# Kernel optimization log

Hardware: AMD Instinct MI355X
Metric: run time of the kernel (lower is better)

Reference implementation:

```python
import jax, jax.numpy as jnp
import numpy as np

EPS = 1e-5
NEG_SLOPE = 0.1


def conv_bn_lrelu(x, w, g, b, rm, rv):
    # 1x1 conv (no bias) + BatchNorm (inference, running stats) + LeakyReLU(0.1)
    # x: [B,C,H,W], w: [O,C]
    y = jnp.einsum('bchw,oc->bohw', x, w)
    scale = g / jnp.sqrt(rv + EPS)
    y = y * scale[None, :, None, None] + (b - rm * scale)[None, :, None, None]
    return jnp.where(y >= 0, y, NEG_SLOPE * y)


def setup_inputs() -> dict:
    key = jax.random.key(0)
    ks = jax.random.split(key, 16)
    B, C, H1, W1, H2, W2 = 4, 256, 32, 32, 64, 64
    C8 = C // 8
    inp = {
        'x1': jax.random.normal(ks[0], (B, C, H1, W1), jnp.float32),
        'x2': jax.random.normal(ks[1], (B, C, H2, W2), jnp.float32),
        'wq': jax.random.normal(ks[2], (C8, C), jnp.float32) * 0.05,
        'wk': jax.random.normal(ks[3], (C8, C), jnp.float32) * 0.05,
        'wv': jax.random.normal(ks[4], (C, C), jnp.float32) * 0.05,
        'gq': jnp.ones((C8,), jnp.float32), 'bq': jnp.zeros((C8,), jnp.float32),
        'mq': jax.random.normal(ks[5], (C8,), jnp.float32) * 0.1,
        'vq': jax.random.uniform(ks[6], (C8,), jnp.float32, 0.5, 1.5),
        'gk': jnp.ones((C8,), jnp.float32), 'bk': jnp.zeros((C8,), jnp.float32),
        'mk': jax.random.normal(ks[7], (C8,), jnp.float32) * 0.1,
        'vk': jax.random.uniform(ks[8], (C8,), jnp.float32, 0.5, 1.5),
        'gv': jnp.ones((C,), jnp.float32), 'bv': jnp.zeros((C,), jnp.float32),
        'mv': jax.random.normal(ks[9], (C,), jnp.float32) * 0.1,
        'vv': jax.random.uniform(ks[10], (C,), jnp.float32, 0.5, 1.5),
        'gamma': jnp.full((1,), 0.5, jnp.float32),
    }
    return inp


def reference(x1, x2, wq, wk, wv, gq, bq, mq, vq, gk, bk, mk, vk, gv, bv, mv, vv, gamma):
    B, C, H2, W2 = x2.shape
    # bilinear upsample x1 to x2's spatial size (align_corners=False == half-pixel)
    x1u = jax.image.resize(x1, (B, C, H2, W2), method='bilinear')
    N = H2 * W2
    q = conv_bn_lrelu(x1u, wq, gq, bq, mq, vq).reshape(B, -1, N)  # [B,C8,N]
    k = conv_bn_lrelu(x2, wk, gk, bk, mk, vk).reshape(B, -1, N)   # [B,C8,N]
    v = conv_bn_lrelu(x2, wv, gv, bv, mv, vv).reshape(B, -1, N)   # [B,C,N]
    energy = jnp.einsum('bdm,bdn->bmn', q, k)                      # [B,N,N]
    attn = jax.nn.softmax(energy, axis=-1)
    out = jnp.einsum('bcn,bmn->bcm', v, attn).reshape(B, C, H2, W2)
    return gamma[0] * out + x1u
```

## Files before the change

kernel.cpp:

```cpp
#include <hip/hip_runtime.h>

#define B_ 4
#define C_ 256
#define N_ 4096
#define LOG2E 1.4426950408889634f

typedef short short8 __attribute__((ext_vector_type(8)));
typedef short short4_ __attribute__((ext_vector_type(4)));
typedef float float4v __attribute__((ext_vector_type(4)));
typedef unsigned int uint2v __attribute__((ext_vector_type(2)));
typedef unsigned int u32;

__device__ inline unsigned short f2b(float x){
  unsigned u = __builtin_bit_cast(unsigned, x);
  u = u + 0x7FFFu + ((u >> 16) & 1u);
  return (unsigned short)(u >> 16);
}

__device__ inline u32 cvtpk(float lo, float hi){
  u32 r; asm("v_cvt_pk_bf16_f32 %0, %1, %2" : "=v"(r) : "v"(lo), "v"(hi)); return r;
}

__device__ inline void gload16(const void* g, void* l){
  __builtin_amdgcn_global_load_lds((const __attribute__((address_space(1))) u32*)g,
                                   (__attribute__((address_space(3))) u32*)l, 16, 0, 0);
}

__global__ void fold_w_kernel(const float* __restrict__ wq, const float* __restrict__ wk,
    const float* __restrict__ wv,
    const float* gq, const float* bq, const float* mq, const float* vq,
    const float* gk, const float* bk, const float* mk, const float* vk,
    const float* gv, const float* bv, const float* mv, const float* vv,
    unsigned short* wqb, unsigned short* wkb, unsigned short* wvb,
    float* biasq, float* biask, float* biasv){
  int i = blockIdx.x*256 + threadIdx.x;
  int o = i >> 8;
  float sv = gv[o]*rsqrtf(vv[o]+1e-5f);
  wvb[i] = f2b(wv[i]*sv);
  if (i < 32*256){
    int oq = i >> 8;
    float sq = gq[oq]*rsqrtf(vq[oq]+1e-5f);
    wqb[i] = f2b(wq[i]*sq*LOG2E);
    float sk = gk[oq]*rsqrtf(vk[oq]+1e-5f);
    wkb[i] = f2b(wk[i]*sk);
  }
  if (i < 256) biasv[i] = bv[i] - mv[i]*(gv[i]*rsqrtf(vv[i]+1e-5f));
  if (i < 32){
    biasq[i] = (bq[i] - mq[i]*(gq[i]*rsqrtf(vq[i]+1e-5f)))*LOG2E;
    biask[i] = bk[i] - mk[i]*(gk[i]*rsqrtf(vk[i]+1e-5f));
  }
}

__global__ __launch_bounds__(256, 2)
void pre_kernel(const float* __restrict__ x1, const float* __restrict__ x2,
                const unsigned short* __restrict__ wqb,
                const unsigned short* __restrict__ wkb,
                const unsigned short* __restrict__ wvb,
                const float* __restrict__ biasq, const float* __restrict__ biask,
                const float* __restrict__ biasv,
                float* __restrict__ x1u,
                unsigned short* __restrict__ Qb, unsigned short* __restrict__ Kb,
                unsigned short* __restrict__ Vb){
  __shared__ unsigned short xt[64*260];
  int b = blockIdx.y;
  int t = threadIdx.x;
  int lane = t&63, w = t>>6, l15 = lane&15, g = lane>>4;

  if (blockIdx.z == 0){
    if (blockIdx.x >= 64) return;
    int y = blockIdx.x;
    float fy = 0.5f*y - 0.25f;
    float y0f = floorf(fy); float wy = fy - y0f;
    int y0 = max(0,min(31,(int)y0f)), y1 = max(0,min(31,(int)y0f+1));
    int x = t & 63, cg = t >> 6;
    float fx = 0.5f*x - 0.25f;
    float x0f = floorf(fx); float wx = fx - x0f;
    int x0 = max(0,min(31,(int)x0f)), x1i = max(0,min(31,(int)x0f+1));
    #pragma unroll 8
    for (int i=0;i<64;i++){
      int c = cg + i*4;
      const float* s0 = x1 + ((size_t)(b*C_ + c)*32 + y0)*32;
      const float* s1 = x1 + ((size_t)(b*C_ + c)*32 + y1)*32;
      float v00=s0[x0], v01=s0[x1i], v10=s1[x0], v11=s1[x1i];
      float v0 = v00 + wx*(v01-v00), v1 = v10 + wx*(v11-v10);
      float val = v0 + wy*(v1-v0);
      x1u[(size_t)(b*C_ + c)*N_ + y*64 + x] = val;
      xt[x*260 + c] = f2b(val);
    }
    __syncthreads();
    const unsigned short* arow = xt + (w*16+l15)*260 + g*8;
    short8 a[8];
    #pragma unroll
    for (int kk=0;kk<8;kk++){
      short4_ lo = *(const short4_*)(arow + kk*32);
      short4_ hi = *(const short4_*)(arow + kk*32 + 4);
      short8 af;
      af[0]=lo[0];af[1]=lo[1];af[2]=lo[2];af[3]=lo[3];
      af[4]=hi[0];af[5]=hi[1];af[6]=hi[2];af[7]=hi[3];
      a[kk]=af;
    }
    #pragma unroll
    for (int ot=0; ot<2; ot++){
      int o = ot*16 + l15;
      const unsigned short* wrow = wqb + o*C_ + g*8;
      float4v acc = {0.f,0.f,0.f,0.f};
      #pragma unroll
      for (int kk=0;kk<8;kk++){
        short8 bf = *(const short8*)(wrow + kk*32);
        acc = __builtin_amdgcn_mfma_f32_16x16x32_bf16(a[kk], bf, acc, 0,0,0);
      }
      float bs = biasq[o];
      #pragma unroll
      for (int r=0;r<4;r++){
        float yv = acc[r] + bs;
        yv = yv >= 0.f ? yv : 0.1f*yv;
        int m = y*64 + w*16 + g*4 + r;
        Qb[(size_t)(b*N_+m)*32 + o] = f2b(yv);
      }
    }
  } else {
    int n0 = blockIdx.x*32;
    int n = t & 31, cg = t >> 5;
    #pragma unroll 8
    for (int i=0;i<32;i++){
      int c = cg + i*8;
      float v = x2[(size_t)(b*C_ + c)*N_ + n0 + n];
      xt[n*260 + c] = f2b(v);
    }
    __syncthreads();
    int mt = w & 1;
    const unsigned short* arow = xt + (mt*16+l15)*260 + g*8;
    short8 a[8];
    #pragma unroll
    for (int kk=0;kk<8;kk++){
      short4_ lo = *(const short4_*)(arow + kk*32);
      short4_ hi = *(const short4_*)(arow + kk*32 + 4);
      short8 af;
      af[0]=lo[0];af[1]=lo[1];af[2]=lo[2];af[3]=lo[3];
      af[4]=hi[0];af[5]=hi[1];af[6]=hi[2];af[7]=hi[3];
      a[kk]=af;
    }
    if (w < 2){
      #pragma unroll
      for (int ot=0; ot<2; ot++){
        int o = ot*16 + l15;
        const unsigned short* wrow = wkb + o*C_ + g*8;
        float4v acc = {0.f,0.f,0.f,0.f};
        #pragma unroll
        for (int kk=0;kk<8;kk++){
          short8 bf = *(const short8*)(wrow + kk*32);
          acc = __builtin_amdgcn_mfma_f32_16x16x32_bf16(a[kk], bf, acc, 0,0,0);
        }
        float bs = biask[o];
        #pragma unroll
        for (int r=0;r<4;r++){
          float yv = acc[r] + bs;
          yv = yv >= 0.f ? yv : 0.1f*yv;
          int m = n0 + w*16 + g*4 + r;
          Kb[(size_t)(b*N_+m)*32 + o] = f2b(yv);
        }
      }
    }
    #pragma unroll
    for (int i=0;i<8;i++){
      int o = ((w>>1)*8 + i)*16 + l15;
      const unsigned short* wrow = wvb + (size_t)o*C_ + g*8;
      float4v acc = {0.f,0.f,0.f,0.f};
      #pragma unroll
      for (int kk=0;kk<8;kk++){
        short8 bf = *(const short8*)(wrow + kk*32);
        acc = __builtin_amdgcn_mfma_f32_16x16x32_bf16(a[kk], bf, acc, 0,0,0);
      }
      float bs = biasv[o];
      #pragma unroll
      for (int r=0;r<4;r++){
        float yv = acc[r] + bs;
        yv = yv >= 0.f ? yv : 0.1f*yv;
        int m = n0 + mt*16 + g*4 + r;
        Vb[(size_t)(b*C_ + o)*N_ + m] = f2b(yv);
      }
    }
  }
}

__global__ __launch_bounds__(512, 2)
void attn_kernel(const unsigned short* __restrict__ Qb,
                 const unsigned short* __restrict__ Kb,
                 const unsigned short* __restrict__ Vb,
                 const float* __restrict__ x1u,
                 const float* __restrict__ gamma_p,
                 float* __restrict__ out){
  __shared__ __align__(16) char smem[74528];
  int* flagsB = (int*)(smem + 73728);
  float* sclB = (float*)(smem + 73760);
  float* lst  = (float*)(smem + 74272);

  int wg = blockIdx.y*64 + blockIdx.x;
  int id = (wg & 7)*32 + (wg >> 3);
  int b = id >> 6, mblk = id & 63;
  int t = threadIdx.x, lane = t & 63, w = t >> 6;
  int l15 = lane & 15, g = lane >> 4;
  int swz = (l15 & 7) << 4;
  int cq = w & 3, ks = w >> 2;

  short8 qf{};
  if (w < 4)
    qf = *(const short8*)(Qb + (size_t)(b*N_ + mblk*64 + w*16 + l15)*32 + g*8);

  float4v acc[4][4];
  #pragma unroll
  for (int mt=0;mt<4;mt++)
    #pragma unroll
    for (int ct=0;ct<4;ct++) acc[mt][ct] = (float4v){0.f,0.f,0.f,0.f};
  float mrow = -1e30f, lrun = 0.f;
  const float4v zero4 = {0.f,0.f,0.f,0.f};

  u32 goff[4]; int loff[4];
  #pragma unroll
  for (int j=0;j<4;j++){
    int i = j*512 + t;
    int c = i >> 3, jj = i & 7;
    loff[j] = i*16;
    goff[j] = (u32)(c*(N_*2)) + (u32)((jj ^ (c & 7)) << 4);
  }
  const char* Vbyte = (const char*)Vb + (size_t)b*C_*N_*2;
  const short* kbase = (const short*)Kb + (size_t)(b*N_ + l15)*32 + g*8;

  auto stageV = [&](int tt, char* buf){
    const char* src = Vbyte + tt*128;
    #pragma unroll
    for (int j=0;j<4;j++) gload16(src + goff[j], buf + loff[j]);
  };
  auto loadK = [&](short8 (&kf)[4], int tt){
    const short* kp = kbase + (size_t)tt*64*32;
    #pragma unroll
    for (int j=0;j<4;j++) kf[j] = *(const short8*)(kp + j*512);
  };

  auto softmaxA = [&](const short8 (&kf)[4], int pdst, uint2v (&pk)[4]){
    float4v s[4];
    #pragma unroll
    for (int j=0;j<4;j++)
      s[j] = __builtin_amdgcn_mfma_f32_16x16x32_bf16(kf[j], qf, zero4, 0, 0, 0);
    float tmax = fmaxf(fmaxf(fmaxf(s[0][0],s[0][1]),fmaxf(s[0][2],s[0][3])),
               fmaxf(fmaxf(fmaxf(s[1][0],s[1][1]),fmaxf(s[1][2],s[1][3])),
               fmaxf(fmaxf(fmaxf(s[2][0],s[2][1]),fmaxf(s[2][2],s[2][3])),
                     fmaxf(fmaxf(s[3][0],s[3][1]),fmaxf(s[3][2],s[3][3])))));
    int trig = __any((tmax > mrow + 8.f) ? 1 : 0) ? 1 : 0;
    if (lane == 0) flagsB[pdst*4 + w] = trig;
    if (trig){
      float tm = fmaxf(tmax, __shfl_xor(tmax, 16));
      tm = fmaxf(tm, __shfl_xor(tm, 32));
      float mnew = fmaxf(mrow, tm);
      float sc = exp2f(mrow - mnew);
      mrow = mnew; lrun *= sc;
      if (lane < 16) sclB[pdst*64 + w*16 + l15] = sc;
    }
    #pragma unroll
    for (int j=0;j<4;j++){
      float p0 = exp2f(s[j][0]-mrow), p1 = exp2f(s[j][1]-mrow);
      float p2 = exp2f(s[j][2]-mrow), p3 = exp2f(s[j][3]-mrow);
      lrun += (p0+p1)+(p2+p3);
      pk[j] = (uint2v){cvtpk(p0, p1), cvtpk(p2, p3)};
    }
  };
  auto softmaxB = [&](uint2v (&pk)[4]){
    char* pw = smem + 65536 + w*2048 + l15*128;
    #pragma unroll
    for (int j=0;j<4;j++)
      *(uint2v*)(pw + ((j*32 + g*8) ^ swz)) = pk[j];
  };

  auto body = [&](int tt, short8 (&kC)[4], short8 (&kN)[4], uint2v (&pk)[4]){
    int pp = tt & 1;
    if (tt < 63) stageV(tt+1, smem + ((tt+1)&1)*32768);
    if (w < 4){
      loadK(kN, (tt+2) & 63);
      if (tt < 63) softmaxA(kC, (tt+1)&1, pk);
    }
    #pragma unroll
    for (int mt=0;mt<4;mt++){
      if (flagsB[pp*4 + mt]){
        float4v sv = *(float4v*)(sclB + pp*64 + mt*16 + g*4);
        #pragma unroll
        for (int ct=0;ct<4;ct++){
          acc[mt][ct][0]*=sv[0]; acc[mt][ct][1]*=sv[1];
          acc[mt][ct][2]*=sv[2]; acc[mt][ct][3]*=sv[3];
        }
      }
    }
    int ko = (ks*64 + g*16) ^ swz;
    char* vbc = smem + (tt&1)*32768;
    short8 pa[4], vf[4];
    #pragma unroll
    for (int mt=0;mt<4;mt++)
      pa[mt] = *(const short8*)(smem + 65536 + mt*2048 + l15*128 + ko);
    #pragma unroll
    for (int ct=0;ct<4;ct++)
      vf[ct] = *(const short8*)(vbc + (cq*64 + ct*16 + l15)*128 + ko);
    __builtin_amdgcn_s_setprio(1);
    #pragma unroll
    for (int mt=0;mt<4;mt++)
      #pragma unroll
      for (int ct=0;ct<4;ct++)
        acc[mt][ct] = __builtin_amdgcn_mfma_f32_16x16x32_bf16(pa[mt], vf[ct], acc[mt][ct], 0, 0, 0);
    __builtin_amdgcn_s_setprio(0);
    __syncthreads();
    if (w < 4 && tt < 63) softmaxB(pk);
    __syncthreads();
  };

  short8 kA[4], kB[4];
  uint2v pkA[4], pkB[4];
  stageV(0, smem);
  if (w < 4){
    short8 k0[4];
    loadK(k0, 0);
    softmaxA(k0, 0, pkA);
    softmaxB(pkA);
    loadK(kA, 1);
  }
  __syncthreads();

  for (int tt=0; tt<64; tt+=2){
    body(tt,   kA, kB, pkA);
    body(tt+1, kB, kA, pkB);
  }

  if (w < 4){
    lrun += __shfl_xor(lrun, 16);
    lrun += __shfl_xor(lrun, 32);
    if (lane < 16) lst[w*16 + l15] = lrun;
  }
  float* cb = (float*)smem + cq*4160;
  if (ks == 1){
    #pragma unroll
    for (int mt=0;mt<4;mt++)
      #pragma unroll
      for (int ct=0;ct<4;ct++)
        #pragma unroll
        for (int r=0;r<4;r++)
          cb[(mt*16 + g*4 + r)*65 + ct*16 + l15] = acc[mt][ct][r];
  }
  __syncthreads();
  if (ks == 0){
    float4v lv[4];
    #pragma unroll
    for (int mt=0;mt<4;mt++) lv[mt] = *(float4v*)(lst + mt*16 + g*4);
    #pragma unroll
    for (int mt=0;mt<4;mt++)
      #pragma unroll
      for (int ct=0;ct<4;ct++)
        #pragma unroll
        for (int r=0;r<4;r++){
          int idx = (mt*16 + g*4 + r)*65 + ct*16 + l15;
          cb[idx] = (acc[mt][ct][r] + cb[idx]) / lv[mt][r];
        }
  }
  __syncthreads();
  float gm = gamma_p[0];
  const float* xr = x1u + (size_t)(b*C_ + cq*64 + ks*32)*N_ + mblk*64;
  float* orow = out + (size_t)(b*C_ + cq*64 + ks*32)*N_ + mblk*64;
  #pragma unroll 8
  for (int i=0; i<32; i++){
    int c_l = ks*32 + i;
    float v = cb[lane*65 + c_l];
    orow[(size_t)i*N_ + lane] = gm*v + xr[(size_t)i*N_ + lane];
  }
}

extern "C" void kernel_launch(void* const* d_in, const int* in_sizes, int n_in,
                              void* d_out, int out_size, void* d_ws, size_t ws_size,
                              hipStream_t stream){
  (void)in_sizes; (void)n_in; (void)out_size; (void)ws_size;
  const float* x1 = (const float*)d_in[0];
  const float* x2 = (const float*)d_in[1];
  const float* wq = (const float*)d_in[2];
  const float* wk = (const float*)d_in[3];
  const float* wv = (const float*)d_in[4];
  const float* gq = (const float*)d_in[5];
  const float* bq = (const float*)d_in[6];
  const float* mq = (const float*)d_in[7];
  const float* vq = (const float*)d_in[8];
  const float* gk = (const float*)d_in[9];
  const float* bk = (const float*)d_in[10];
  const float* mk = (const float*)d_in[11];
  const float* vk = (const float*)d_in[12];
  const float* gv = (const float*)d_in[13];
  const float* bv = (const float*)d_in[14];
  const float* mv = (const float*)d_in[15];
  const float* vv = (const float*)d_in[16];
  const float* gamma = (const float*)d_in[17];
  float* out = (float*)d_out;

  char* p = (char*)d_ws;
  float* x1u          = (float*)p;          p += (size_t)B_*C_*N_*4;
  unsigned short* Qb  = (unsigned short*)p; p += (size_t)B_*N_*32*2;
  unsigned short* Kb  = (unsigned short*)p; p += (size_t)B_*N_*32*2;
  unsigned short* Vb  = (unsigned short*)p; p += (size_t)B_*C_*N_*2;
  unsigned short* wqb = (unsigned short*)p; p += 32*256*2;
  unsigned short* wkb = (unsigned short*)p; p += 32*256*2;
  unsigned short* wvb = (unsigned short*)p; p += 256*256*2;
  float* biasq        = (float*)p;          p += 32*4;
  float* biask        = (float*)p;          p += 32*4;
  float* biasv        = (float*)p;          p += 256*4;

  fold_w_kernel<<<256, 256, 0, stream>>>(wq,wk,wv,gq,bq,mq,vq,gk,bk,mk,vk,gv,bv,mv,vv,
                                         wqb,wkb,wvb,biasq,biask,biasv);
  pre_kernel<<<dim3(128,4,2), 256, 0, stream>>>(x1, x2, wqb, wkb, wvb,
                                                biasq, biask, biasv, x1u, Qb, Kb, Vb);
  attn_kernel<<<dim3(64,4), 512, 0, stream>>>(Qb, Kb, Vb, x1u, gamma, out);
}
```

Measured before the change: 125.6 us.

## Split attention key range across two wave groups per block with softmax merge

Doubles the attention block to 1024 threads, organised as two independent groups of 8 waves. Each group processes half of the key/value sequence with its own double-buffered V staging and P tile in LDS. At the end, the two groups' running max and sum statistics are merged flash-decoding style, and their partial outputs are combined with rescaling factors. This halves the sequential loop length per block and raises waves per CU, aiming to hide latency better. The cost is much larger LDS usage (about 151 KB) and an extra cross-group reduction step.

```diff
diff --git a/kernel.cpp b/kernel.cpp
--- a/kernel.cpp
+++ b/kernel.cpp
@@ -183,29 +183,31 @@
   }
 }
 
-__global__ __launch_bounds__(512, 2)
+__global__ __launch_bounds__(1024, 2)
 void attn_kernel(const unsigned short* __restrict__ Qb,
                  const unsigned short* __restrict__ Kb,
                  const unsigned short* __restrict__ Vb,
                  const float* __restrict__ x1u,
                  const float* __restrict__ gamma_p,
                  float* __restrict__ out){
-  __shared__ __align__(16) char smem[74528];
-  int* flagsB = (int*)(smem + 73728);
-  float* sclB = (float*)(smem + 73760);
-  float* lst  = (float*)(smem + 74272);
+  __shared__ __align__(16) char smem[151424];
+  int* flagsB  = (int*)(smem + 147456);
+  float* sclB  = (float*)(smem + 147520);
+  float* stats = (float*)(smem + 149568);
+  float* facL  = (float*)(smem + 150592);
 
   int wg = blockIdx.y*64 + blockIdx.x;
   int id = (wg & 7)*32 + (wg >> 3);
   int b = id >> 6, mblk = id & 63;
   int t = threadIdx.x, lane = t & 63, w = t >> 6;
+  int ng = w >> 3, wl = w & 7;
   int l15 = lane & 15, g = lane >> 4;
   int swz = (l15 & 7) << 4;
-  int cq = w & 3, ks = w >> 2;
+  int cq = wl & 3, ks = wl >> 2;
 
   short8 qf{};
-  if (w < 4)
-    qf = *(const short8*)(Qb + (size_t)(b*N_ + mblk*64 + w*16 + l15)*32 + g*8);
+  if (wl < 4)
+    qf = *(const short8*)(Qb + (size_t)(b*N_ + mblk*64 + wl*16 + l15)*32 + g*8);
 
   float4v acc[4][4];
   #pragma unroll
@@ -216,23 +218,24 @@
   const float4v zero4 = {0.f,0.f,0.f,0.f};
 
   u32 goff[4]; int loff[4];
+  int lt = t & 511;
   #pragma unroll
   for (int j=0;j<4;j++){
-    int i = j*512 + t;
+    int i = j*512 + lt;
     int c = i >> 3, jj = i & 7;
-    loff[j] = i*16;
+    loff[j] = ng*65536 + i*16;
     goff[j] = (u32)(c*(N_*2)) + (u32)((jj ^ (c & 7)) << 4);
   }
-  const char* Vbyte = (const char*)Vb + (size_t)b*C_*N_*2;
-  const short* kbase = (const short*)Kb + (size_t)(b*N_ + l15)*32 + g*8;
-
-  auto stageV = [&](int tt, char* buf){
-    const char* src = Vbyte + tt*128;
-    #pragma unroll
-    for (int j=0;j<4;j++) gload16(src + goff[j], buf + loff[j]);
+  const char* Vbyte = (const char*)Vb + (size_t)b*C_*N_*2 + ng*4096;
+  const short* kbase = (const short*)Kb + (size_t)(b*N_ + ng*2048 + l15)*32 + g*8;
+
+  auto stageV = [&](int ttl, int par){
+    const char* src = Vbyte + ttl*128;
+    #pragma unroll
+    for (int j=0;j<4;j++) gload16(src + goff[j], smem + loff[j] + par*32768);
   };
-  auto loadK = [&](short8 (&kf)[4], int tt){
-    const short* kp = kbase + (size_t)tt*64*32;
+  auto loadK = [&](short8 (&kf)[4], int ttl){
+    const short* kp = kbase + (size_t)ttl*64*32;
     #pragma unroll
     for (int j=0;j<4;j++) kf[j] = *(const short8*)(kp + j*512);
   };
@@ -247,14 +250,14 @@
                fmaxf(fmaxf(fmaxf(s[2][0],s[2][1]),fmaxf(s[2][2],s[2][3])),
                      fmaxf(fmaxf(s[3][0],s[3][1]),fmaxf(s[3][2],s[3][3])))));
     int trig = __any((tmax > mrow + 8.f) ? 1 : 0) ? 1 : 0;
-    if (lane == 0) flagsB[pdst*4 + w] = trig;
+    if (lane == 0) flagsB[pdst*8 + ng*4 + wl] = trig;
     if (trig){
       float tm = fmaxf(tmax, __shfl_xor(tmax, 16));
       tm = fmaxf(tm, __shfl_xor(tm, 32));
       float mnew = fmaxf(mrow, tm);
       float sc = exp2f(mrow - mnew);
       mrow = mnew; lrun *= sc;
-      if (lane < 16) sclB[pdst*64 + w*16 + l15] = sc;
+      if (lane < 16) sclB[(pdst*2 + ng)*64 + wl*16 + l15] = sc;
     }
     #pragma unroll
     for (int j=0;j<4;j++){
@@ -265,7 +268,7 @@
     }
   };
   auto softmaxB = [&](uint2v (&pk)[4]){
-    char* pw = smem + 65536 + w*2048 + l15*128;
+    char* pw = smem + 131072 + ng*8192 + wl*2048 + l15*128;
     #pragma unroll
     for (int j=0;j<4;j++)
       *(uint2v*)(pw + ((j*32 + g*8) ^ swz)) = pk[j];
@@ -273,15 +276,15 @@
 
   auto body = [&](int tt, short8 (&kC)[4], short8 (&kN)[4], uint2v (&pk)[4]){
     int pp = tt & 1;
-    if (tt < 63) stageV(tt+1, smem + ((tt+1)&1)*32768);
-    if (w < 4){
-      loadK(kN, (tt+2) & 63);
-      if (tt < 63) softmaxA(kC, (tt+1)&1, pk);
+    if (tt < 31) stageV(tt+1, (tt+1)&1);
+    if (wl < 4){
+      loadK(kN, (tt+2) & 31);
+      if (tt < 31) softmaxA(kC, (tt+1)&1, pk);
     }
     #pragma unroll
     for (int mt=0;mt<4;mt++){
-      if (flagsB[pp*4 + mt]){
-        float4v sv = *(float4v*)(sclB + pp*64 + mt*16 + g*4);
+      if (flagsB[pp*8 + ng*4 + mt]){
+        float4v sv = *(float4v*)(sclB + (pp*2+ng)*64 + mt*16 + g*4);
         #pragma unroll
         for (int ct=0;ct<4;ct++){
           acc[mt][ct][0]*=sv[0]; acc[mt][ct][1]*=sv[1];
@@ -290,11 +293,12 @@
       }
     }
     int ko = (ks*64 + g*16) ^ swz;
-    char* vbc = smem + (tt&1)*32768;
+    char* vbc = smem + ng*65536 + (tt&1)*32768;
+    const char* pbase = smem + 131072 + ng*8192;
     short8 pa[4], vf[4];
     #pragma unroll
     for (int mt=0;mt<4;mt++)
-      pa[mt] = *(const short8*)(smem + 65536 + mt*2048 + l15*128 + ko);
+      pa[mt] = *(const short8*)(pbase + mt*2048 + l15*128 + ko);
     #pragma unroll
     for (int ct=0;ct<4;ct++)
       vf[ct] = *(const short8*)(vbc + (cq*64 + ct*16 + l15)*128 + ko);
@@ -306,14 +310,14 @@
         acc[mt][ct] = __builtin_amdgcn_mfma_f32_16x16x32_bf16(pa[mt], vf[ct], acc[mt][ct], 0, 0, 0);
     __builtin_amdgcn_s_setprio(0);
     __syncthreads();
-    if (w < 4 && tt < 63) softmaxB(pk);
+    if (wl < 4 && tt < 31) softmaxB(pk);
     __syncthreads();
   };
 
   short8 kA[4], kB[4];
   uint2v pkA[4], pkB[4];
-  stageV(0, smem);
-  if (w < 4){
+  stageV(0, 0);
+  if (wl < 4){
     short8 k0[4];
     loadK(k0, 0);
     softmaxA(k0, 0, pkA);
@@ -322,17 +326,20 @@
   }
   __syncthreads();
 
-  for (int tt=0; tt<64; tt+=2){
+  for (int tt=0; tt<32; tt+=2){
     body(tt,   kA, kB, pkA);
     body(tt+1, kB, kA, pkB);
   }
 
-  if (w < 4){
+  if (wl < 4){
     lrun += __shfl_xor(lrun, 16);
     lrun += __shfl_xor(lrun, 32);
-    if (lane < 16) lst[w*16 + l15] = lrun;
-  }
-  float* cb = (float*)smem + cq*4160;
+    if (lane < 16){
+      stats[(ng*64 + wl*16 + l15)*2    ] = mrow;
+      stats[(ng*64 + wl*16 + l15)*2 + 1] = lrun;
+    }
+  }
+  float* cbg = (float*)smem + ng*16640 + cq*4160;
   if (ks == 1){
     #pragma unroll
     for (int mt=0;mt<4;mt++)
@@ -340,32 +347,39 @@
       for (int ct=0;ct<4;ct++)
         #pragma unroll
         for (int r=0;r<4;r++)
-          cb[(mt*16 + g*4 + r)*65 + ct*16 + l15] = acc[mt][ct][r];
+          cbg[(mt*16 + g*4 + r)*65 + ct*16 + l15] = acc[mt][ct][r];
   }
   __syncthreads();
+  if (t < 64){
+    float m0s = stats[t*2],        l0 = stats[t*2 + 1];
+    float m1s = stats[(64+t)*2],   l1 = stats[(64+t)*2 + 1];
+    float M = fmaxf(m0s, m1s);
+    float f0 = exp2f(m0s - M), f1 = exp2f(m1s - M);
+    float L = l0*f0 + l1*f1;
+    facL[t] = f0; facL[64+t] = f1; facL[128+t] = 1.f/L;
+  }
   if (ks == 0){
-    float4v lv[4];
-    #pragma unroll
-    for (int mt=0;mt<4;mt++) lv[mt] = *(float4v*)(lst + mt*16 + g*4);
     #pragma unroll
     for (int mt=0;mt<4;mt++)
       #pragma unroll
       for (int ct=0;ct<4;ct++)
         #pragma unroll
-        for (int r=0;r<4;r++){
-          int idx = (mt*16 + g*4 + r)*65 + ct*16 + l15;
-          cb[idx] = (acc[mt][ct][r] + cb[idx]) / lv[mt][r];
-        }
+        for (int r=0;r<4;r++)
+          cbg[(mt*16 + g*4 + r)*65 + ct*16 + l15] += acc[mt][ct][r];
   }
   __syncthreads();
   float gm = gamma_p[0];
-  const float* xr = x1u + (size_t)(b*C_ + cq*64 + ks*32)*N_ + mblk*64;
-  float* orow = out + (size_t)(b*C_ + cq*64 + ks*32)*N_ + mblk*64;
+  const float* cb0 = (float*)smem + cq*4160;
+  const float* cb1 = cb0 + 16640;
+  float fw0 = facL[lane]*facL[128+lane]*gm;
+  float fw1 = facL[64+lane]*facL[128+lane]*gm;
+  const float* xr = x1u + (size_t)(b*C_ + cq*64)*N_ + mblk*64;
+  float* orow = out + (size_t)(b*C_ + cq*64)*N_ + mblk*64;
   #pragma unroll 8
-  for (int i=0; i<32; i++){
-    int c_l = ks*32 + i;
-    float v = cb[lane*65 + c_l];
-    orow[(size_t)i*N_ + lane] = gm*v + xr[(size_t)i*N_ + lane];
+  for (int i=0; i<16; i++){
+    int c_l = ks*32 + ng*16 + i;
+    float v = cb0[lane*65 + c_l]*fw0 + cb1[lane*65 + c_l]*fw1;
+    orow[(size_t)c_l*N_ + lane] = v + xr[(size_t)c_l*N_ + lane];
   }
 }
 
@@ -409,5 +423,5 @@
                                          wqb,wkb,wvb,biasq,biask,biasv);
   pre_kernel<<<dim3(128,4,2), 256, 0, stream>>>(x1, x2, wqb, wkb, wvb,
                                                 biasq, biask, biasv, x1u, Qb, Kb, Vb);
-  attn_kernel<<<dim3(64,4), 512, 0, stream>>>(Qb, Kb, Vb, x1u, gamma, out);
-}
+  attn_kernel<<<dim3(64,4), 1024, 0, stream>>>(Qb, Kb, Vb, x1u, gamma, out);
+}
```

Measured after the change: 280.9 us. 2.24x slower.
